# Kernel optimization log

Hardware: AMD Instinct MI355X
Metric: run time of the kernel (lower is better)

The kernel has to match this reference:

```python
import jax, jax.numpy as jnp
import numpy as np

D = 1024
H = 8
HD = D // H
SCALE = HD ** -0.5


def setup_inputs() -> dict:
    key = jax.random.key(0)
    ks = jax.random.split(key, 12)
    s = 0.02
    return {
        "x": jax.random.normal(ks[0], (4, 2048, D), dtype=jnp.float32),
        "attn_mask": jax.random.randint(ks[1], (2048, 2048), 0, 2, dtype=jnp.int32),
        "qkv_w": jax.random.normal(ks[2], (3 * D, D), dtype=jnp.float32) * s,
        "qkv_b": jnp.zeros((3 * D,), dtype=jnp.float32),
        "q_w": jax.random.normal(ks[3], (D, D), dtype=jnp.float32) * s,
        "q_b": jnp.zeros((D,), dtype=jnp.float32),
        "k_w": jax.random.normal(ks[4], (D, D), dtype=jnp.float32) * s,
        "k_b": jnp.zeros((D,), dtype=jnp.float32),
        "v_w": jax.random.normal(ks[5], (D, D), dtype=jnp.float32) * s,
        "v_b": jnp.zeros((D,), dtype=jnp.float32),
        "out_w": jax.random.normal(ks[6], (D, D), dtype=jnp.float32) * s,
        "out_b": jnp.zeros((D,), dtype=jnp.float32),
    }


def reference(x, attn_mask, qkv_w, qkv_b, q_w, q_b, k_w, k_b, v_w, v_b, out_w, out_b):
    B, S, _ = x.shape
    qkv = x @ qkv_w.T + qkv_b
    q, k, v = jnp.split(qkv, 3, axis=-1)
    # per-stream multi-head projections, then split heads: [B,H,S,HD]
    def heads(t, w, b):
        return (t @ w.T + b).reshape(B, S, H, HD).transpose(0, 2, 1, 3)
    q = heads(q, q_w, q_b)
    k = heads(k, k_w, k_b)
    v = heads(v, v_w, v_b)
    # scaled dot-product attention with masked softmax
    scores = jnp.einsum("bhqd,bhkd->bhqk", q, k) * SCALE
    scores = jnp.where(attn_mask == 1, -jnp.inf, scores)
    attn = jax.nn.softmax(scores, axis=-1)
    o = jnp.einsum("bhqk,bhkd->bhqd", attn, v)
    o = o.transpose(0, 2, 1, 3).reshape(B, S, D)
    return o @ out_w.T + out_b
```

## Files before the change

kernel.cpp:

```cpp
#include <hip/hip_runtime.h>
#include <stdint.h>

typedef unsigned short u16;
typedef unsigned int u32;
typedef unsigned long long u64;
using f32x4 = __attribute__((ext_vector_type(4))) float;
using f32x16 = __attribute__((ext_vector_type(16))) float;
using s16x8 = __attribute__((ext_vector_type(8))) short;
using u16x4 = __attribute__((ext_vector_type(4))) unsigned short;
using u32x4 = __attribute__((ext_vector_type(4))) u32;

static constexpr float kQScale = (float)(0.08838834764831845 * 1.4426950408889634);

__device__ __forceinline__ u16 f2bf(float f) {
  uint32_t u = __float_as_uint(f);
  u += 0x7fffu + ((u >> 16) & 1u);
  return (u16)(u >> 16);
}

__device__ __forceinline__ float fexp2(float x) {
#if __has_builtin(__builtin_amdgcn_exp2f)
  return __builtin_amdgcn_exp2f(x);
#else
  return exp2f(x);
#endif
}

__device__ __forceinline__ u32 cvtpk(float lo, float hi) {
  u32 r;
  asm("v_cvt_pk_bf16_f32 %0, %1, %2" : "=v"(r) : "v"(lo), "v"(hi));
  return r;
}

__device__ __forceinline__ void mfma16(f32x4& d, s16x8 a, s16x8 b) {
  asm volatile("v_mfma_f32_16x16x32_bf16 %0, %1, %2, %0" : "+v"(d) : "v"(a), "v"(b));
}
__device__ __forceinline__ void mfma32(f32x16& d, s16x8 a, s16x8 b) {
  asm volatile("v_mfma_f32_32x32x16_bf16 %0, %1, %2, %0" : "+v"(d) : "v"(a), "v"(b));
}
__device__ __forceinline__ f32x16 mfma32_z(s16x8 a, s16x8 b) {
  f32x16 d;
  asm volatile("v_mfma_f32_32x32x16_bf16 %0, %1, %2, 0" : "=&v"(d) : "v"(a), "v"(b));
  return d;
}

__device__ __forceinline__ void g2lds16(const void* g, void* l) {
  __builtin_amdgcn_global_load_lds(
      (__attribute__((address_space(1))) void*)(uintptr_t)g,
      (__attribute__((address_space(3))) void*)(uint32_t)(uintptr_t)l, 16, 0, 0);
}

#define BAR() asm volatile("s_barrier" ::: "memory")

__global__ __launch_bounds__(256) void cvt_f32_bf16(const float* __restrict__ in,
                                                    u16* __restrict__ out, int n) {
  int i = (blockIdx.x * 256 + threadIdx.x) * 4;
  if (i + 3 < n) {
    f32x4 v = *(const f32x4*)(in + i);
    u16x4 o = {f2bf(v.x), f2bf(v.y), f2bf(v.z), f2bf(v.w)};
    *(u16x4*)(out + i) = o;
  }
}

__global__ __launch_bounds__(256) void cvt4(const float* __restrict__ a, const float* __restrict__ b,
                                            const float* __restrict__ c, const float* __restrict__ d,
                                            u16* __restrict__ out) {
  int z = blockIdx.y;
  const float* in = z == 0 ? a : z == 1 ? b : z == 2 ? c : d;
  int i = (blockIdx.x * 256 + threadIdx.x) * 4;
  f32x4 v = *(const f32x4*)(in + i);
  u16x4 o = {f2bf(v.x), f2bf(v.y), f2bf(v.z), f2bf(v.w)};
  *(u16x4*)(out + (size_t)z * 1048576 + i) = o;
}

__global__ __launch_bounds__(256) void transpose_f32_bf16(const float* __restrict__ in,
                                                          u16* __restrict__ out, int R, int C) {
  __shared__ u16 tile[32][33];
  int bx = blockIdx.x, by = blockIdx.y;
  int tx = threadIdx.x & 31, ty = threadIdx.x >> 5;
#pragma unroll
  for (int k = 0; k < 4; ++k)
    tile[ty + k * 8][tx] = f2bf(in[(size_t)(by * 32 + ty + k * 8) * C + bx * 32 + tx]);
  __syncthreads();
#pragma unroll
  for (int k = 0; k < 4; ++k)
    out[(size_t)(bx * 32 + ty + k * 8) * R + by * 32 + tx] = tile[tx][ty + k * 8];
}

__global__ __launch_bounds__(256) void cbias3(const float* __restrict__ qw, const float* __restrict__ kw,
                                              const float* __restrict__ vw, const float* __restrict__ qkvb,
                                              const float* __restrict__ qb, const float* __restrict__ kb,
                                              const float* __restrict__ vb, float* __restrict__ out) {
  int z = blockIdx.y;
  const float* w = z == 0 ? qw : (z == 1 ? kw : vw);
  const float* ba = z == 0 ? qb : (z == 1 ? kb : vb);
  const float* bi = qkvb + z * 1024;
  int o = blockIdx.x * 4 + (threadIdx.x >> 6);
  int lane = threadIdx.x & 63;
  float s = 0.f;
  for (int m = lane; m < 1024; m += 64) s += w[o * 1024 + m] * bi[m];
#pragma unroll
  for (int d = 1; d < 64; d <<= 1) s += __shfl_xor(s, d);
  if (lane == 0) {
    float fin = s + ba[o];
    if (z == 0) fin *= kQScale;
    out[z * 1024 + o] = fin;
  }
}

__global__ __launch_bounds__(256) void pack_mask(const int* __restrict__ m, u64* __restrict__ pm) {
  int row = blockIdx.x;
  int wv = threadIdx.x >> 6, lane = threadIdx.x & 63;
#pragma unroll
  for (int i = 0; i < 8; ++i) {
    int word = wv * 8 + i;
    u64 b = __ballot(m[(size_t)row * 2048 + word * 64 + lane] == 0);
    if (lane == 0) pm[(size_t)row * 32 + word] = b;
  }
}

template <typename OUT_T, bool BIAS_PER_ROW>
__global__ __launch_bounds__(256, 2) void gemm_nt(const u16* __restrict__ A, int lda, long bsA,
                                                  const u16* __restrict__ B, int ldb, long bsB,
                                                  OUT_T* __restrict__ C, int ldc, long bsC,
                                                  const float* __restrict__ bias, long bsBias,
                                                  int NtilesN, int K, float scale_z0) {
  __shared__ __align__(16) u16 As[128 * 64];
  __shared__ __align__(16) u16 Bs[128 * 64];
  const int z = blockIdx.z;
  const float sc = (z == 0) ? scale_z0 : 1.f;
  A += (size_t)z * bsA; B += (size_t)z * bsB; C += (size_t)z * bsC;
  if (bias) bias += (size_t)z * bsBias;
  const int tm = blockIdx.x / NtilesN, tn = blockIdx.x % NtilesN;
  const int tid = threadIdx.x, lane = tid & 63, w = tid >> 6;
  const int wm = w >> 1, wn = w & 1;
  const int q = lane & 15, g = lane >> 4;
  f32x4 acc[4][4] = {};

  const u16* Ab = A + (size_t)(tm * 128 + (tid >> 3)) * lda + ((tid & 7) << 3);
  const u16* Bb = B + (size_t)(tn * 128 + (tid >> 3)) * ldb + ((tid & 7) << 3);
  char* AsW = (char*)As + (w << 10);
  char* BsW = (char*)Bs + (w << 10);

  for (int k0 = 0; k0 < K; k0 += 64) {
#pragma unroll
    for (int it = 0; it < 4; ++it) {
      g2lds16(Ab + (size_t)(it * 32) * lda + k0, AsW + it * 4096);
      g2lds16(Bb + (size_t)(it * 32) * ldb + k0, BsW + it * 4096);
    }
    __syncthreads();
#pragma unroll
    for (int kk = 0; kk < 2; ++kk) {
      s16x8 af[4], bf[4];
#pragma unroll
      for (int i = 0; i < 4; ++i)
        af[i] = *(const s16x8*)((const char*)As + (wm * 64 + i * 16 + q) * 128 + kk * 64 + g * 16);
#pragma unroll
      for (int i = 0; i < 4; ++i)
        bf[i] = *(const s16x8*)((const char*)Bs + (wn * 64 + i * 16 + q) * 128 + kk * 64 + g * 16);
#pragma unroll
      for (int mf = 0; mf < 4; ++mf)
#pragma unroll
        for (int nf = 0; nf < 4; ++nf) mfma16(acc[mf][nf], af[mf], bf[nf]);
    }
    __syncthreads();
  }
  asm volatile("s_nop 7\n\ts_nop 7");
#pragma unroll
  for (int mf = 0; mf < 4; ++mf)
#pragma unroll
    for (int nf = 0; nf < 4; ++nf) {
      const int row = tm * 128 + wm * 64 + mf * 16 + g * 4;
      const int col = tn * 128 + wn * 64 + nf * 16 + q;
      float bc = (!BIAS_PER_ROW && bias) ? bias[col] : 0.f;
#pragma unroll
      for (int r = 0; r < 4; ++r) {
        float v = acc[mf][nf][r] * sc;
        if (bias) v += BIAS_PER_ROW ? bias[row + r] : bc;
        if constexpr (sizeof(OUT_T) == 2)
          C[(size_t)(row + r) * ldc + col] = (OUT_T)f2bf(v);
        else
          C[(size_t)(row + r) * ldc + col] = (OUT_T)v;
      }
    }
}

__global__ __launch_bounds__(512, 1) void gemm256(const u16* __restrict__ A, int lda,
                                                  const u16* __restrict__ B, int ldb,
                                                  u16* __restrict__ C, int ldc,
                                                  const float* __restrict__ bias,
                                                  int K, int NtN) {
  __shared__ __align__(16) u16 Als[2][256 * 64];
  __shared__ __align__(16) u16 Bls[2][256 * 64];
  const int bid = blockIdx.x;
  const int cpx = gridDim.x >> 3;
  const int wgid = (bid & 7) * cpx + (bid >> 3);
  const int tm = wgid / NtN, tn = wgid % NtN;
  const int tid = threadIdx.x, lane = tid & 63, w = tid >> 6;
  const int wm = w >> 2, wn = w & 3;
  const int q = lane & 15, g = lane >> 4, qk = q & 7;
  const int nT = K >> 6;

  f32x4 acc[8][4] = {};
  s16x8 af[4][2], bf[4][2];

  const int srow = tid >> 3, sch = tid & 7;
  const int gcol = (sch ^ (srow & 7)) << 3;
  const u16* Abase = A + (size_t)(tm * 256 + srow) * lda + gcol;
  const u16* Bbase = B + (size_t)(tn * 256 + srow) * ldb + gcol;

  auto stageA = [&](int buf, int kt, int h) {
    const u16* s0 = Abase + (size_t)(h * 128) * lda + (kt << 6);
    char* d = (char*)&Als[buf][0] + h * 16384 + (w << 10);
    g2lds16(s0, d);
    g2lds16(s0 + (size_t)64 * lda, d + 8192);
  };
  auto stageB = [&](int buf, int kt, int h) {
    const u16* s0 = Bbase + (size_t)(h * 128) * ldb + (kt << 6);
    char* d = (char*)&Bls[buf][0] + h * 16384 + (w << 10);
    g2lds16(s0, d);
    g2lds16(s0 + (size_t)64 * ldb, d + 8192);
  };
  auto loadA = [&](const char* base, int mh) {
#pragma unroll
    for (int mf = 0; mf < 4; ++mf)
#pragma unroll
      for (int kk = 0; kk < 2; ++kk)
        af[mf][kk] = *(const s16x8*)(base + (mh * 128 + wm * 64 + mf * 16 + q) * 128 +
                                     ((((kk << 2) + g) ^ qk) << 4));
  };
  auto loadB = [&](const char* base, int nh) {
#pragma unroll
    for (int nf = 0; nf < 2; ++nf)
#pragma unroll
      for (int kk = 0; kk < 2; ++kk)
        bf[nh * 2 + nf][kk] = *(const s16x8*)(base + (nh * 128 + wn * 32 + nf * 16 + q) * 128 +
                                              ((((kk << 2) + g) ^ qk) << 4));
  };
  auto quad = [&](int mh, int nh) {
    __builtin_amdgcn_s_setprio(1);
#pragma unroll
    for (int mf = 0; mf < 4; ++mf)
#pragma unroll
      for (int nf = 0; nf < 2; ++nf)
#pragma unroll
        for (int kk = 0; kk < 2; ++kk)
          mfma16(acc[mh * 4 + mf][nh * 2 + nf], af[mf][kk], bf[nh * 2 + nf][kk]);
    __builtin_amdgcn_s_setprio(0);
  };

  stageA(0, 0, 0); stageA(0, 0, 1); stageB(0, 0, 0); stageB(0, 0, 1);
  const int kt1 = (1 < nT) ? 1 : 0;
  stageB(1, kt1, 0); stageB(1, kt1, 1);
  asm volatile("s_waitcnt vmcnt(4)" ::: "memory");
  BAR();

  for (int kt = 0; kt < nT; ++kt) {
    const int buf = kt & 1;
    const char* Ab = (const char*)&Als[buf][0];
    const char* Bb = (const char*)&Bls[buf][0];
    const int ktA = (kt + 1 < nT) ? kt + 1 : nT - 1;
    const int ktB = (kt + 2 < nT) ? kt + 2 : nT - 1;
    loadA(Ab, 0); loadB(Bb, 0);
    stageA(buf ^ 1, ktA, 0);
    BAR();
    quad(0, 0);
    BAR();
    loadB(Bb, 1);
    stageA(buf ^ 1, ktA, 1);
    BAR();
    quad(0, 1);
    asm volatile("s_waitcnt vmcnt(8)" ::: "memory");
    BAR();
    loadA(Ab, 1);
    stageB(buf, ktB, 0);
    BAR();
    quad(1, 0);
    BAR();
    stageB(buf, ktB, 1);
    BAR();
    quad(1, 1);
    asm volatile("s_waitcnt vmcnt(6)" ::: "memory");
    BAR();
  }

  asm volatile("s_nop 7\n\ts_nop 7");
#pragma unroll
  for (int mf = 0; mf < 8; ++mf) {
    const int row = tm * 256 + (mf >> 2) * 128 + wm * 64 + (mf & 3) * 16 + g * 4;
#pragma unroll
    for (int nf = 0; nf < 4; ++nf) {
      const int col = tn * 256 + (nf >> 1) * 128 + wn * 32 + (nf & 1) * 16 + q;
      const float bc = bias[col];
#pragma unroll
      for (int r = 0; r < 4; ++r)
        C[(size_t)(row + r) * ldc + col] = f2bf(acc[mf][nf][r] + bc);
    }
  }
}

__global__ __launch_bounds__(256, 2) void attn_fwd(const u16* __restrict__ Qb, const u16* __restrict__ Kb,
                                                   int ldq, const u16* __restrict__ Vt,
                                                   const u64* __restrict__ pmask,
                                                   u16* __restrict__ Ob) {
  __shared__ __align__(16) char K_lds[2][16384];
  __shared__ __align__(16) char V_lds[3][16384];
  const int n = blockIdx.x;
  const int slot = n >> 3;
  const int grp = (n & 7) * 4 + (slot >> 4);
  const int qt = slot & 15;
  const int h = grp & 7, b = grp >> 3;
  const int tid = threadIdx.x, w = tid >> 6, lane = tid & 63;
  const int ql = lane & 31;
  const int hi = lane >> 5;
  const int q0 = qt * 128;

  s16x8 qf[8];
  const u16* qrow = Qb + (size_t)(b * 2048 + q0 + w * 32 + ql) * ldq + h * 128 + 8 * hi;
#pragma unroll
  for (int kd = 0; kd < 8; ++kd) qf[kd] = *(const s16x8*)(qrow + 16 * kd);

  u32x4 ov = {0x3F803F80u, 0x3F803F80u, 0x3F803F80u, 0x3F803F80u};
  const s16x8 ones = __builtin_bit_cast(s16x8, ov);

  f32x16 oacc[4] = {};
  f32x16 lacc = {};

  const int ksr = tid >> 4, ksc = tid & 15;
  const int vsr = tid >> 3, vsc = tid & 7;
  const int sw = ql & 15;
  const u64* pmrow = pmask + (size_t)(q0 + w * 32 + ql) * 32;

  auto stageK = [&](int buf, int s2) {
    const int kv0 = s2 * 64;
    char* kb = K_lds[buf] + (w << 10);
#pragma unroll
    for (int it = 0; it < 4; ++it) {
      int kr = it * 16 + ksr;
      g2lds16(Kb + (size_t)(b * 2048 + kv0 + kr) * ldq + h * 128 + ((ksc ^ (kr & 15)) << 3),
              kb + it * 4096);
    }
  };
  auto stageV = [&](int buf, int s2) {
    const int kv0 = s2 * 64;
    char* vb = V_lds[buf] + (w << 10);
#pragma unroll
    for (int it = 0; it < 4; ++it) {
      int vr = it * 32 + vsr;
      g2lds16(Vt + (size_t)(h * 128 + vr) * 8192 + b * 2048 + kv0 + ((vsc ^ (vr & 7)) << 3),
              vb + it * 4096);
    }
  };
  auto qk = [&](f32x16& d0, f32x16& d1, int kbuf) {
    const char* Kc = K_lds[kbuf];
#pragma unroll
    for (int kd = 0; kd < 8; ++kd) {
      int c = (2 * kd + hi) ^ sw;
      s16x8 kf0 = *(const s16x8*)(Kc + ql * 256 + (c << 4));
      s16x8 kf1 = *(const s16x8*)(Kc + (32 + ql) * 256 + (c << 4));
      if (kd == 0) { d0 = mfma32_z(kf0, qf[0]); d1 = mfma32_z(kf1, qf[0]); }
      else         { mfma32(d0, kf0, qf[kd]);   mfma32(d1, kf1, qf[kd]); }
    }
  };

  auto body = [&](f32x16& c0, f32x16& c1, f32x16& n0, f32x16& n1, int s, int vbR, int vbW) {
    u64 pw = pmrow[s];
    const int sc2 = (s + 2 < 32) ? s + 2 : 31;
    stageK(s & 1, sc2);
    stageV(vbW, sc2);
    if (s + 1 < 32) qk(n0, n1, (s + 1) & 1);
    const char* Vc = V_lds[vbR];
    s16x8 pa[2];
#pragma unroll
    for (int half = 0; half < 2; ++half) {
      u32 halfm = (u32)(pw >> (32 * half + 4 * hi));
      u32 Wp[4][2];
#pragma unroll
      for (int t = 0; t < 4; ++t) {
        float e[4];
#pragma unroll
        for (int j = 0; j < 4; ++j) {
          float ev = fexp2(half == 0 ? c0[4 * t + j] : c1[4 * t + j]);
          int km;
          asm("v_bfe_i32 %0, %1, %2, 1" : "=v"(km) : "v"(halfm), "n"(8 * t + j));
          e[j] = __uint_as_float(__float_as_uint(ev) & (u32)km);
        }
        Wp[t][0] = cvtpk(e[0], e[1]);
        Wp[t][1] = cvtpk(e[2], e[3]);
      }
#pragma unroll
      for (int kq = 0; kq < 2; ++kq) {
        u32 s0 = hi ? Wp[2 * kq][0] : Wp[2 * kq + 1][0];
        u32 s1 = hi ? Wp[2 * kq][1] : Wp[2 * kq + 1][1];
        u32 r0 = (u32)__shfl_xor((int)s0, 32);
        u32 r1 = (u32)__shfl_xor((int)s1, 32);
        u32 o0 = hi ? Wp[2 * kq + 1][0] : Wp[2 * kq][0];
        u32 o1 = hi ? Wp[2 * kq + 1][1] : Wp[2 * kq][1];
        u32x4 wv;
        wv.x = hi ? r0 : o0;
        wv.y = hi ? r1 : o1;
        wv.z = hi ? o0 : r0;
        wv.w = hi ? o1 : r1;
        pa[kq] = __builtin_bit_cast(s16x8, wv);
      }
      asm volatile("s_nop 3");
      __builtin_amdgcn_s_setprio(1);
#pragma unroll
      for (int kq = 0; kq < 2; ++kq) {
        const int ks = 2 * half + kq;
#pragma unroll
        for (int dt = 0; dt < 4; ++dt) {
          int vrow = dt * 32 + ql;
          s16x8 vf = *(const s16x8*)(Vc + vrow * 128 + (((2 * ks + hi) ^ (vrow & 7)) << 4));
          mfma32(oacc[dt], pa[kq], vf);
        }
        mfma32(lacc, pa[kq], ones);
      }
      __builtin_amdgcn_s_setprio(0);
    }
    asm volatile("s_waitcnt vmcnt(4)" ::: "memory");
    BAR();
  };

  stageK(0, 0); stageV(0, 0); stageK(1, 1); stageV(1, 1);
  asm volatile("s_waitcnt vmcnt(4)" ::: "memory");
  BAR();
  f32x16 sA0, sA1, sB0, sB1;
  qk(sA0, sA1, 0);
  BAR();

  int vb = 0;
  for (int s2 = 0; s2 < 16; ++s2) {
    const int s = 2 * s2;
    const int vb1 = (vb + 1 == 3) ? 0 : vb + 1;
    const int vb2 = (vb + 2 >= 3) ? vb - 1 : vb + 2;
    body(sA0, sA1, sB0, sB1, s, vb, vb2);
    body(sB0, sB1, sA0, sA1, s + 1, vb1, vb);
    vb = vb2;
  }

  asm volatile("s_nop 7\n\ts_nop 7");
#pragma unroll
  for (int dt = 0; dt < 4; ++dt)
#pragma unroll
    for (int reg = 0; reg < 16; ++reg) {
      int qr = (reg & 3) + 8 * (reg >> 2) + 4 * hi;
      size_t trow = (size_t)(b * 2048 + q0 + w * 32 + qr);
      Ob[trow * 1024 + h * 128 + dt * 32 + ql] = f2bf(oacc[dt][reg] / lacc[reg]);
    }
}

extern "C" void kernel_launch(void* const* d_in, const int* in_sizes, int n_in,
                              void* d_out, int out_size, void* d_ws, size_t ws_size,
                              hipStream_t stream) {
  (void)in_sizes; (void)n_in; (void)out_size; (void)ws_size;
  const float* x    = (const float*)d_in[0];
  const int*   am   = (const int*)d_in[1];
  const float* qkvw = (const float*)d_in[2];
  const float* qkvb = (const float*)d_in[3];
  const float* qw   = (const float*)d_in[4];
  const float* qb   = (const float*)d_in[5];
  const float* kw   = (const float*)d_in[6];
  const float* kb   = (const float*)d_in[7];
  const float* vw   = (const float*)d_in[8];
  const float* vb   = (const float*)d_in[9];
  const float* ow   = (const float*)d_in[10];
  const float* ob   = (const float*)d_in[11];

  char* p = (char*)d_ws;
  auto take = [&](size_t n) { char* r = p; p += (n + 255) & ~(size_t)255; return r; };
  u16* xb    = (u16*)take(8192ull * 1024 * 2);
  u16* qkvwT = (u16*)take(1024ull * 3072 * 2);
  u16* wb4   = (u16*)take(4ull * 1048576 * 2);
  u16* comb3 = (u16*)take(3ull * 1048576 * 2);
  float* cb3 = (float*)take(3ull * 1024 * 4);
  u16* QK2   = (u16*)take(8192ull * 2048 * 2);
  u16* V2t   = (u16*)take(8192ull * 1024 * 2);
  u64* pm    = (u64*)take(2048ull * 32 * 8);
  u16* Obuf  = xb;

  cvt_f32_bf16<<<8192, 256, 0, stream>>>(x, xb, 8192 * 1024);
  cvt4<<<dim3(1024, 4), 256, 0, stream>>>(qw, kw, vw, ow, wb4);
  transpose_f32_bf16<<<dim3(32, 96), 256, 0, stream>>>(qkvw, qkvwT, 3072, 1024);
  cbias3<<<dim3(256, 3), 256, 0, stream>>>(qw, kw, vw, qkvb, qb, kb, vb, cb3);

  gemm_nt<u16, false><<<dim3(64, 1, 3), 256, 0, stream>>>(
      wb4, 1024, 1048576, qkvwT, 3072, 1024, comb3, 1024, 1048576, nullptr, 0, 8, 1024, kQScale);
  gemm256<<<256, 512, 0, stream>>>(xb, 1024, comb3, 1024, QK2, 2048, cb3, 1024, 8);
  gemm_nt<u16, true><<<dim3(512, 1, 1), 256, 0, stream>>>(
      comb3 + 2 * 1048576, 1024, 0, xb, 1024, 0, V2t, 8192, 0, cb3 + 2048, 0, 64, 1024, 1.f);

  pack_mask<<<2048, 256, 0, stream>>>(am, pm);
  attn_fwd<<<512, 256, 0, stream>>>(QK2, QK2 + 1024, 2048, V2t, pm, Obuf);

  gemm_nt<float, false><<<dim3(512, 1, 1), 256, 0, stream>>>(
      Obuf, 1024, 0, wb4 + 3 * 1048576, 1024, 0, (float*)d_out, 1024, 0, ob, 0, 8, 1024, 1.f);
}
```

Before: 243.7 us.

## Merge prep kernels into one launch and fold V projection into 256-tile GEMM

Folds the five small preprocessing kernels (x cast, weight casts, qkv_w transpose, combined bias, mask packing) into a single block-indexed prep kernel. The separate 128-tile V-transposed GEMM is also merged into the 256x256 gemm256 kernel, which now runs 384 workgroups: 256 for Q/K and 128 for V^T, with per-row bias for the V tiles. This removes several launch gaps and gives the V projection the larger, pipelined tile path. In exchange the GEMM is specialized to fixed shapes, and grid rasterization now mixes Q/K and V tiles.

New measurement: 258.0 us. +5.9%, slower.

```diff
diff --git a/kernel.cpp b/kernel.cpp
--- a/kernel.cpp
+++ b/kernel.cpp
@@ -52,70 +52,67 @@
 
 #define BAR() asm volatile("s_barrier" ::: "memory")
 
-__global__ __launch_bounds__(256) void cvt_f32_bf16(const float* __restrict__ in,
-                                                    u16* __restrict__ out, int n) {
-  int i = (blockIdx.x * 256 + threadIdx.x) * 4;
-  if (i + 3 < n) {
+__global__ __launch_bounds__(256) void prep(const float* __restrict__ x, u16* __restrict__ xb,
+                                            const float* __restrict__ qw, const float* __restrict__ kw,
+                                            const float* __restrict__ vw, const float* __restrict__ ow,
+                                            u16* __restrict__ wb4,
+                                            const float* __restrict__ qkvw, u16* __restrict__ qkvwT,
+                                            const float* __restrict__ qkvb, const float* __restrict__ qb,
+                                            const float* __restrict__ kb, const float* __restrict__ vb,
+                                            float* __restrict__ cb3,
+                                            const int* __restrict__ am, u64* __restrict__ pm) {
+  __shared__ u16 tile[32][33];
+  const int bid = blockIdx.x, tid = threadIdx.x;
+  if (bid < 8192) {
+    int i = (bid * 256 + tid) * 4;
+    f32x4 v = *(const f32x4*)(x + i);
+    u16x4 o = {f2bf(v.x), f2bf(v.y), f2bf(v.z), f2bf(v.w)};
+    *(u16x4*)(xb + i) = o;
+  } else if (bid < 12288) {
+    int idx = bid - 8192;
+    int z = idx >> 10;
+    const float* in = z == 0 ? qw : z == 1 ? kw : z == 2 ? vw : ow;
+    int i = ((idx & 1023) * 256 + tid) * 4;
     f32x4 v = *(const f32x4*)(in + i);
     u16x4 o = {f2bf(v.x), f2bf(v.y), f2bf(v.z), f2bf(v.w)};
-    *(u16x4*)(out + i) = o;
-  }
-}
-
-__global__ __launch_bounds__(256) void cvt4(const float* __restrict__ a, const float* __restrict__ b,
-                                            const float* __restrict__ c, const float* __restrict__ d,
-                                            u16* __restrict__ out) {
-  int z = blockIdx.y;
-  const float* in = z == 0 ? a : z == 1 ? b : z == 2 ? c : d;
-  int i = (blockIdx.x * 256 + threadIdx.x) * 4;
-  f32x4 v = *(const f32x4*)(in + i);
-  u16x4 o = {f2bf(v.x), f2bf(v.y), f2bf(v.z), f2bf(v.w)};
-  *(u16x4*)(out + (size_t)z * 1048576 + i) = o;
-}
-
-__global__ __launch_bounds__(256) void transpose_f32_bf16(const float* __restrict__ in,
-                                                          u16* __restrict__ out, int R, int C) {
-  __shared__ u16 tile[32][33];
-  int bx = blockIdx.x, by = blockIdx.y;
-  int tx = threadIdx.x & 31, ty = threadIdx.x >> 5;
-#pragma unroll
-  for (int k = 0; k < 4; ++k)
-    tile[ty + k * 8][tx] = f2bf(in[(size_t)(by * 32 + ty + k * 8) * C + bx * 32 + tx]);
-  __syncthreads();
-#pragma unroll
-  for (int k = 0; k < 4; ++k)
-    out[(size_t)(bx * 32 + ty + k * 8) * R + by * 32 + tx] = tile[tx][ty + k * 8];
-}
-
-__global__ __launch_bounds__(256) void cbias3(const float* __restrict__ qw, const float* __restrict__ kw,
-                                              const float* __restrict__ vw, const float* __restrict__ qkvb,
-                                              const float* __restrict__ qb, const float* __restrict__ kb,
-                                              const float* __restrict__ vb, float* __restrict__ out) {
-  int z = blockIdx.y;
-  const float* w = z == 0 ? qw : (z == 1 ? kw : vw);
-  const float* ba = z == 0 ? qb : (z == 1 ? kb : vb);
-  const float* bi = qkvb + z * 1024;
-  int o = blockIdx.x * 4 + (threadIdx.x >> 6);
-  int lane = threadIdx.x & 63;
-  float s = 0.f;
-  for (int m = lane; m < 1024; m += 64) s += w[o * 1024 + m] * bi[m];
-#pragma unroll
-  for (int d = 1; d < 64; d <<= 1) s += __shfl_xor(s, d);
-  if (lane == 0) {
-    float fin = s + ba[o];
-    if (z == 0) fin *= kQScale;
-    out[z * 1024 + o] = fin;
-  }
-}
-
-__global__ __launch_bounds__(256) void pack_mask(const int* __restrict__ m, u64* __restrict__ pm) {
-  int row = blockIdx.x;
-  int wv = threadIdx.x >> 6, lane = threadIdx.x & 63;
-#pragma unroll
-  for (int i = 0; i < 8; ++i) {
-    int word = wv * 8 + i;
-    u64 b = __ballot(m[(size_t)row * 2048 + word * 64 + lane] == 0);
-    if (lane == 0) pm[(size_t)row * 32 + word] = b;
+    *(u16x4*)(wb4 + (size_t)z * 1048576 + i) = o;
+  } else if (bid < 15360) {
+    int idx = bid - 12288;
+    int bx = idx & 31, by = idx >> 5;
+    int tx = tid & 31, ty = tid >> 5;
+#pragma unroll
+    for (int k = 0; k < 4; ++k)
+      tile[ty + k * 8][tx] = f2bf(qkvw[(size_t)(by * 32 + ty + k * 8) * 1024 + bx * 32 + tx]);
+    __syncthreads();
+#pragma unroll
+    for (int k = 0; k < 4; ++k)
+      qkvwT[(size_t)(bx * 32 + ty + k * 8) * 3072 + by * 32 + tx] = tile[tx][ty + k * 8];
+  } else if (bid < 16128) {
+    int idx = bid - 15360;
+    int z = idx >> 8;
+    const float* w = z == 0 ? qw : (z == 1 ? kw : vw);
+    const float* ba = z == 0 ? qb : (z == 1 ? kb : vb);
+    const float* bi = qkvb + z * 1024;
+    int o = (idx & 255) * 4 + (tid >> 6);
+    int lane = tid & 63;
+    float s = 0.f;
+    for (int m = lane; m < 1024; m += 64) s += w[o * 1024 + m] * bi[m];
+#pragma unroll
+    for (int d = 1; d < 64; d <<= 1) s += __shfl_xor(s, d);
+    if (lane == 0) {
+      float fin = s + ba[o];
+      if (z == 0) fin *= kQScale;
+      cb3[z * 1024 + o] = fin;
+    }
+  } else {
+    int row = bid - 16128;
+    int wv = tid >> 6, lane = tid & 63;
+#pragma unroll
+    for (int i = 0; i < 8; ++i) {
+      int word = wv * 8 + i;
+      u64 b = __ballot(am[(size_t)row * 2048 + word * 64 + lane] == 0);
+      if (lane == 0) pm[(size_t)row * 32 + word] = b;
+    }
   }
 }
 
@@ -185,21 +182,34 @@
     }
 }
 
-__global__ __launch_bounds__(512, 1) void gemm256(const u16* __restrict__ A, int lda,
-                                                  const u16* __restrict__ B, int ldb,
-                                                  u16* __restrict__ C, int ldc,
-                                                  const float* __restrict__ bias,
-                                                  int K, int NtN) {
+__global__ __launch_bounds__(512, 1) void gemm256_qkv(const u16* __restrict__ xb,
+                                                      const u16* __restrict__ comb3,
+                                                      const float* __restrict__ cb3,
+                                                      u16* __restrict__ QK2,
+                                                      u16* __restrict__ V2t) {
   __shared__ __align__(16) u16 Als[2][256 * 64];
   __shared__ __align__(16) u16 Bls[2][256 * 64];
   const int bid = blockIdx.x;
   const int cpx = gridDim.x >> 3;
   const int wgid = (bid & 7) * cpx + (bid >> 3);
-  const int tm = wgid / NtN, tn = wgid % NtN;
+  const bool isV = wgid >= 256;
+  const u16 *A, *B;
+  u16* C;
+  const float* bias;
+  int lda, ldb, ldc, tm, tn;
+  if (!isV) {
+    tm = wgid >> 3; tn = wgid & 7;
+    A = xb; lda = 1024; B = comb3; ldb = 1024; C = QK2; ldc = 2048; bias = cb3;
+  } else {
+    int id = wgid - 256;
+    tm = id >> 5; tn = id & 31;
+    A = comb3 + 2 * 1048576; lda = 1024; B = xb; ldb = 1024; C = V2t; ldc = 8192;
+    bias = cb3 + 2048;
+  }
   const int tid = threadIdx.x, lane = tid & 63, w = tid >> 6;
   const int wm = w >> 2, wn = w & 3;
   const int q = lane & 15, g = lane >> 4, qk = q & 7;
-  const int nT = K >> 6;
+  const int nT = 16;
 
   f32x4 acc[8][4] = {};
   s16x8 af[4][2], bf[4][2];
@@ -250,8 +260,7 @@
   };
 
   stageA(0, 0, 0); stageA(0, 0, 1); stageB(0, 0, 0); stageB(0, 0, 1);
-  const int kt1 = (1 < nT) ? 1 : 0;
-  stageB(1, kt1, 0); stageB(1, kt1, 1);
+  stageB(1, 1, 0); stageB(1, 1, 1);
   asm volatile("s_waitcnt vmcnt(4)" ::: "memory");
   BAR();
 
@@ -291,10 +300,12 @@
 #pragma unroll
     for (int nf = 0; nf < 4; ++nf) {
       const int col = tn * 256 + (nf >> 1) * 128 + wn * 32 + (nf & 1) * 16 + q;
-      const float bc = bias[col];
-#pragma unroll
-      for (int r = 0; r < 4; ++r)
-        C[(size_t)(row + r) * ldc + col] = f2bf(acc[mf][nf][r] + bc);
+      const float bc = isV ? 0.f : bias[col];
+#pragma unroll
+      for (int r = 0; r < 4; ++r) {
+        float v = acc[mf][nf][r] + (isV ? bias[row + r] : bc);
+        C[(size_t)(row + r) * ldc + col] = f2bf(v);
+      }
     }
   }
 }
@@ -479,20 +490,12 @@
   u64* pm    = (u64*)take(2048ull * 32 * 8);
   u16* Obuf  = xb;
 
-  cvt_f32_bf16<<<8192, 256, 0, stream>>>(x, xb, 8192 * 1024);
-  cvt4<<<dim3(1024, 4), 256, 0, stream>>>(qw, kw, vw, ow, wb4);
-  transpose_f32_bf16<<<dim3(32, 96), 256, 0, stream>>>(qkvw, qkvwT, 3072, 1024);
-  cbias3<<<dim3(256, 3), 256, 0, stream>>>(qw, kw, vw, qkvb, qb, kb, vb, cb3);
-
+  prep<<<18176, 256, 0, stream>>>(x, xb, qw, kw, vw, ow, wb4, qkvw, qkvwT,
+                                  qkvb, qb, kb, vb, cb3, am, pm);
   gemm_nt<u16, false><<<dim3(64, 1, 3), 256, 0, stream>>>(
       wb4, 1024, 1048576, qkvwT, 3072, 1024, comb3, 1024, 1048576, nullptr, 0, 8, 1024, kQScale);
-  gemm256<<<256, 512, 0, stream>>>(xb, 1024, comb3, 1024, QK2, 2048, cb3, 1024, 8);
-  gemm_nt<u16, true><<<dim3(512, 1, 1), 256, 0, stream>>>(
-      comb3 + 2 * 1048576, 1024, 0, xb, 1024, 0, V2t, 8192, 0, cb3 + 2048, 0, 64, 1024, 1.f);
-
-  pack_mask<<<2048, 256, 0, stream>>>(am, pm);
+  gemm256_qkv<<<384, 512, 0, stream>>>(xb, comb3, cb3, QK2, V2t);
   attn_fwd<<<512, 256, 0, stream>>>(QK2, QK2 + 1024, 2048, V2t, pm, Obuf);
-
   gemm_nt<float, false><<<dim3(512, 1, 1), 256, 0, stream>>>(
       Obuf, 1024, 0, wb4 + 3 * 1048576, 1024, 0, (float*)d_out, 1024, 0, ob, 0, 8, 1024, 1.f);
 }
```
